# Performance work log

Hardware: AMD Instinct MI355X
Metric: run time of the kernel (lower is better)

The kernel has to match this reference:

```python
import jax, jax.numpy as jnp
import numpy as np

B, C, H, W = 8, 16, 64, 64
O = 32
K = 3
STRIDE = 1
HO = (H - K) // STRIDE + 1  # 62
WO = (W - K) // STRIDE + 1  # 62
BIAS_VAL = 0.1


def setup_inputs() -> dict:
    key = jax.random.key(0)
    k1, k2 = jax.random.split(key)
    x = jax.random.normal(k1, (B, C, H, W), dtype=jnp.float32)
    # per-location weights: (1, O, C, Ho, Wo, K*K) in torch; drop leading 1
    weight = jax.random.normal(k2, (O, C, HO, WO, K * K), dtype=jnp.float32)
    bias = jnp.full((1, O, HO, WO), BIAS_VAL, dtype=jnp.float32)
    return {"x": x, "weight": weight, "bias": bias}


def _extract_patches(x):
    # emulate x.unfold(2,K,S).unfold(3,K,S).reshape(..., K*K)
    # patch index k = ki*K + kj
    patches = [
        x[:, :, ki:ki + (HO - 1) * STRIDE + 1:STRIDE, kj:kj + (WO - 1) * STRIDE + 1:STRIDE]
        for ki in range(K) for kj in range(K)
    ]
    return jnp.stack(patches, axis=-1)  # [B, C, Ho, Wo, K*K]


def reference(x, weight, bias):
    patches = _extract_patches(x)  # [B, C, Ho, Wo, K2]
    # (x.unsqueeze(1) * weight).sum([2, -1]) == contraction over C and K2 per location
    out = jnp.einsum('bchwk,ochwk->bohw', patches, weight)
    return out + bias
```

## Files before the change

kernel.cpp:

```cpp
#include <hip/hip_runtime.h>


#define BB 8
#define CC 16
#define HH 64
#define WW 64
#define OO 32
#define HO 62
#define WO 62
#define NLOC (HO * WO)
#define TOTAL (OO * NLOC)

__device__ __forceinline__ void async_f32_to_lds(const float* g, float* l) {
  __builtin_amdgcn_global_load_lds((const __attribute__((address_space(1))) void*)g,
                                   (__attribute__((address_space(3))) void*)l,
                                   4, 0, 0);
}

__global__ __launch_bounds__(256) void lc2d_kernel(
    const float* __restrict__ x, const float* __restrict__ weight,
    const float* __restrict__ bias, float* __restrict__ out) {
  __shared__ float smem[4 * 2 * 576];

  const int tid  = threadIdx.x;
  const int lane = tid & 63;
  const int wave = tid >> 6;
  const int ho = blockIdx.x % HO;
  const int o  = blockIdx.x / HO;

  float* buf0 = smem + wave * 1152;
  float* buf1 = buf0 + 576;

  const int a1 = ((lane + 1) & 63) << 2;
  const int a2 = ((lane + 2) & 63) << 2;
  const int lidx = (lane < WO ? lane : WO - 1) * 9;

  const float* wbase = weight + (size_t)(o * CC + wave * 4) * (NLOC * 9)
                              + (size_t)ho * (WO * 9);

#pragma unroll
  for (int j = 0; j < 9; ++j) {
    if (j * 64 + lane < WO * 9)
      async_f32_to_lds(wbase + j * 64 + lane, buf0 + j * 64);
  }

  float acc[BB];
#pragma unroll
  for (int b = 0; b < BB; ++b) acc[b] = 0.0f;

  const float* xw = x + (size_t)(wave * 4) * (HH * WW) + (size_t)ho * WW + lane;

  __syncthreads();

  float* cur = buf0;
  float* nxt = buf1;

  for (int cc = 0; cc < 4; ++cc) {
    if (cc < 3) {
      const float* wg = wbase + (size_t)(cc + 1) * (NLOC * 9);
#pragma unroll
      for (int j = 0; j < 9; ++j) {
        if (j * 64 + lane < WO * 9)
          async_f32_to_lds(wg + j * 64 + lane, nxt + j * 64);
      }
    }

    float wreg[9];
#pragma unroll
    for (int k = 0; k < 9; ++k) wreg[k] = cur[lidx + k];

    const float* xc = xw + (size_t)cc * (HH * WW);

    float v[4][3];
#pragma unroll
    for (int b = 0; b < 4; ++b) {
      const float* xb = xc + (size_t)b * (CC * HH * WW);
      v[b][0] = xb[0]; v[b][1] = xb[WW]; v[b][2] = xb[2 * WW];
    }
#pragma unroll
    for (int b = 0; b < 4; ++b) {
      float p01 = __int_as_float(__builtin_amdgcn_ds_bpermute(a1, __float_as_int(v[b][0])));
      float p02 = __int_as_float(__builtin_amdgcn_ds_bpermute(a2, __float_as_int(v[b][0])));
      float p11 = __int_as_float(__builtin_amdgcn_ds_bpermute(a1, __float_as_int(v[b][1])));
      float p12 = __int_as_float(__builtin_amdgcn_ds_bpermute(a2, __float_as_int(v[b][1])));
      float p21 = __int_as_float(__builtin_amdgcn_ds_bpermute(a1, __float_as_int(v[b][2])));
      float p22 = __int_as_float(__builtin_amdgcn_ds_bpermute(a2, __float_as_int(v[b][2])));
      acc[b] += v[b][0] * wreg[0] + p01 * wreg[1] + p02 * wreg[2]
              + v[b][1] * wreg[3] + p11 * wreg[4] + p12 * wreg[5]
              + v[b][2] * wreg[6] + p21 * wreg[7] + p22 * wreg[8];
    }

#pragma unroll
    for (int b = 0; b < 4; ++b) {
      const float* xb = xc + (size_t)(b + 4) * (CC * HH * WW);
      v[b][0] = xb[0]; v[b][1] = xb[WW]; v[b][2] = xb[2 * WW];
    }
#pragma unroll
    for (int b = 0; b < 4; ++b) {
      float p01 = __int_as_float(__builtin_amdgcn_ds_bpermute(a1, __float_as_int(v[b][0])));
      float p02 = __int_as_float(__builtin_amdgcn_ds_bpermute(a2, __float_as_int(v[b][0])));
      float p11 = __int_as_float(__builtin_amdgcn_ds_bpermute(a1, __float_as_int(v[b][1])));
      float p12 = __int_as_float(__builtin_amdgcn_ds_bpermute(a2, __float_as_int(v[b][1])));
      float p21 = __int_as_float(__builtin_amdgcn_ds_bpermute(a1, __float_as_int(v[b][2])));
      float p22 = __int_as_float(__builtin_amdgcn_ds_bpermute(a2, __float_as_int(v[b][2])));
      acc[b + 4] += v[b][0] * wreg[0] + p01 * wreg[1] + p02 * wreg[2]
                  + v[b][1] * wreg[3] + p11 * wreg[4] + p12 * wreg[5]
                  + v[b][2] * wreg[6] + p21 * wreg[7] + p22 * wreg[8];
    }

    __syncthreads();
    float* t = cur; cur = nxt; nxt = t;
  }

#pragma unroll
  for (int b = 0; b < BB; ++b) buf0[lane * 9 + b] = acc[b];
  __syncthreads();

  for (int p = tid; p < 512; p += 256) {
    int b = p >> 6;
    int l = p & 63;
    if (l < WO) {
      float s = smem[0 * 1152 + l * 9 + b] + smem[1 * 1152 + l * 9 + b]
              + smem[2 * 1152 + l * 9 + b] + smem[3 * 1152 + l * 9 + b];
      int loc = o * NLOC + ho * WO + l;
      out[(size_t)b * TOTAL + loc] = s + bias[loc];
    }
  }
}

extern "C" void kernel_launch(void* const* d_in, const int* in_sizes, int n_in,
                              void* d_out, int out_size, void* d_ws, size_t ws_size,
                              hipStream_t stream) {
  const float* x = (const float*)d_in[0];
  const float* w = (const float*)d_in[1];
  const float* bias = (const float*)d_in[2];
  float* out = (float*)d_out;

  hipLaunchKernelGGL(lc2d_kernel, dim3(OO * HO), dim3(256), 0, stream,
                     x, w, bias, out);
}
```

Before: 30.81 us.

## Remap lanes to 4 output columns by 2 batches with vector loads

Each lane now computes 4 adjacent output columns for 2 batches instead of one column for all 8 batches. Weights are read from LDS as float4 and input rows as float4 plus float2 vector loads, which replaces the per-element ds_bpermute neighbour exchange. The final reduction layout in LDS also changes to a contiguous batch-by-column form. This cuts LDS permute traffic and the number of global load instructions, at the cost of more registers and lanes at the edge reading some redundant or padded columns.

```diff
diff --git a/kernel.cpp b/kernel.cpp
--- a/kernel.cpp
+++ b/kernel.cpp
@@ -10,6 +10,9 @@
 #define WO 62
 #define NLOC (HO * WO)
 #define TOTAL (OO * NLOC)
+
+typedef float f4 __attribute__((ext_vector_type(4)));
+typedef float f2 __attribute__((ext_vector_type(2)));
 
 __device__ __forceinline__ void async_f32_to_lds(const float* g, float* l) {
   __builtin_amdgcn_global_load_lds((const __attribute__((address_space(1))) void*)g,
@@ -25,30 +28,28 @@
   const int tid  = threadIdx.x;
   const int lane = tid & 63;
   const int wave = tid >> 6;
+  const int l = lane & 15;
+  const int q = lane >> 4;
   const int ho = blockIdx.x % HO;
   const int o  = blockIdx.x / HO;
 
   float* buf0 = smem + wave * 1152;
   float* buf1 = buf0 + 576;
 
-  const int a1 = ((lane + 1) & 63) << 2;
-  const int a2 = ((lane + 2) & 63) << 2;
-  const int lidx = (lane < WO ? lane : WO - 1) * 9;
+  const int colbase = 4 * l;
+  const int f2off = (l < 15) ? 4 : -4;
 
   const float* wbase = weight + (size_t)(o * CC + wave * 4) * (NLOC * 9)
                               + (size_t)ho * (WO * 9);
 
 #pragma unroll
-  for (int j = 0; j < 9; ++j) {
+  for (int j = 0; j < 9; ++j)
     if (j * 64 + lane < WO * 9)
       async_f32_to_lds(wbase + j * 64 + lane, buf0 + j * 64);
-  }
 
-  float acc[BB];
-#pragma unroll
-  for (int b = 0; b < BB; ++b) acc[b] = 0.0f;
-
-  const float* xw = x + (size_t)(wave * 4) * (HH * WW) + (size_t)ho * WW + lane;
+  f4 acc[2];
+  acc[0] = (f4)0.f;
+  acc[1] = (f4)0.f;
 
   __syncthreads();
 
@@ -59,53 +60,45 @@
     if (cc < 3) {
       const float* wg = wbase + (size_t)(cc + 1) * (NLOC * 9);
 #pragma unroll
-      for (int j = 0; j < 9; ++j) {
+      for (int j = 0; j < 9; ++j)
         if (j * 64 + lane < WO * 9)
           async_f32_to_lds(wg + j * 64 + lane, nxt + j * 64);
-      }
     }
 
-    float wreg[9];
+    f4 wq[9];
 #pragma unroll
-    for (int k = 0; k < 9; ++k) wreg[k] = cur[lidx + k];
+    for (int k = 0; k < 9; ++k)
+      wq[k] = *(const f4*)(cur + 36 * l + 4 * k);
 
-    const float* xc = xw + (size_t)cc * (HH * WW);
-
-    float v[4][3];
-#pragma unroll
-    for (int b = 0; b < 4; ++b) {
-      const float* xb = xc + (size_t)b * (CC * HH * WW);
-      v[b][0] = xb[0]; v[b][1] = xb[WW]; v[b][2] = xb[2 * WW];
-    }
-#pragma unroll
-    for (int b = 0; b < 4; ++b) {
-      float p01 = __int_as_float(__builtin_amdgcn_ds_bpermute(a1, __float_as_int(v[b][0])));
-      float p02 = __int_as_float(__builtin_amdgcn_ds_bpermute(a2, __float_as_int(v[b][0])));
-      float p11 = __int_as_float(__builtin_amdgcn_ds_bpermute(a1, __float_as_int(v[b][1])));
-      float p12 = __int_as_float(__builtin_amdgcn_ds_bpermute(a2, __float_as_int(v[b][1])));
-      float p21 = __int_as_float(__builtin_amdgcn_ds_bpermute(a1, __float_as_int(v[b][2])));
-      float p22 = __int_as_float(__builtin_amdgcn_ds_bpermute(a2, __float_as_int(v[b][2])));
-      acc[b] += v[b][0] * wreg[0] + p01 * wreg[1] + p02 * wreg[2]
-              + v[b][1] * wreg[3] + p11 * wreg[4] + p12 * wreg[5]
-              + v[b][2] * wreg[6] + p21 * wreg[7] + p22 * wreg[8];
-    }
+    const int c = wave * 4 + cc;
 
 #pragma unroll
-    for (int b = 0; b < 4; ++b) {
-      const float* xb = xc + (size_t)(b + 4) * (CC * HH * WW);
-      v[b][0] = xb[0]; v[b][1] = xb[WW]; v[b][2] = xb[2 * WW];
-    }
+    for (int bo = 0; bo < 2; ++bo) {
+      const int b = 2 * q + bo;
+      const float* xb = x + ((size_t)b * CC + c) * (HH * WW)
+                          + (size_t)ho * WW + colbase;
+      f4 v4[3];
+      f2 v2[3];
 #pragma unroll
-    for (int b = 0; b < 4; ++b) {
-      float p01 = __int_as_float(__builtin_amdgcn_ds_bpermute(a1, __float_as_int(v[b][0])));
-      float p02 = __int_as_float(__builtin_amdgcn_ds_bpermute(a2, __float_as_int(v[b][0])));
-      float p11 = __int_as_float(__builtin_amdgcn_ds_bpermute(a1, __float_as_int(v[b][1])));
-      float p12 = __int_as_float(__builtin_amdgcn_ds_bpermute(a2, __float_as_int(v[b][1])));
-      float p21 = __int_as_float(__builtin_amdgcn_ds_bpermute(a1, __float_as_int(v[b][2])));
-      float p22 = __int_as_float(__builtin_amdgcn_ds_bpermute(a2, __float_as_int(v[b][2])));
-      acc[b + 4] += v[b][0] * wreg[0] + p01 * wreg[1] + p02 * wreg[2]
-                  + v[b][1] * wreg[3] + p11 * wreg[4] + p12 * wreg[5]
-                  + v[b][2] * wreg[6] + p21 * wreg[7] + p22 * wreg[8];
+      for (int r = 0; r < 3; ++r) {
+        v4[r] = *(const f4*)(xb + r * WW);
+        v2[r] = *(const f2*)(xb + r * WW + f2off);
+      }
+#pragma unroll
+      for (int w4 = 0; w4 < 4; ++w4) {
+        float s = 0.f;
+#pragma unroll
+        for (int r = 0; r < 3; ++r) {
+#pragma unroll
+          for (int j = 0; j < 3; ++j) {
+            const int e = w4 + j;
+            const int wi = w4 * 9 + r * 3 + j;
+            const float xv = (e < 4) ? v4[r][e] : v2[r][e - 4];
+            s += xv * wq[wi >> 2][wi & 3];
+          }
+        }
+        acc[bo][w4] += s;
+      }
     }
 
     __syncthreads();
@@ -113,16 +106,17 @@
   }
 
 #pragma unroll
-  for (int b = 0; b < BB; ++b) buf0[lane * 9 + b] = acc[b];
+  for (int bo = 0; bo < 2; ++bo)
+    *(f4*)(buf0 + (2 * q + bo) * 64 + colbase) = acc[bo];
   __syncthreads();
 
   for (int p = tid; p < 512; p += 256) {
-    int b = p >> 6;
-    int l = p & 63;
-    if (l < WO) {
-      float s = smem[0 * 1152 + l * 9 + b] + smem[1 * 1152 + l * 9 + b]
-              + smem[2 * 1152 + l * 9 + b] + smem[3 * 1152 + l * 9 + b];
-      int loc = o * NLOC + ho * WO + l;
+    const int b  = p >> 6;
+    const int wo = p & 63;
+    if (wo < WO) {
+      float s = smem[0 * 1152 + p] + smem[1 * 1152 + p]
+              + smem[2 * 1152 + p] + smem[3 * 1152 + p];
+      const int loc = o * NLOC + ho * WO + wo;
       out[(size_t)b * TOTAL + loc] = s + bias[loc];
     }
   }
```

Result: faster. 26.61 us (-13.6%).
